# Optimization experiments

Measured on AMD Instinct MI355X. Metric: run time of the kernel, lower is better.

Reference implementation:

```python
import jax, jax.numpy as jnp
import numpy as np

SIZE = 1024
CODE_DIM = 256
B, H, W = 32, 32, 32


def setup_inputs() -> dict:
    key = jax.random.key(0)
    k1, k2 = jax.random.split(key)
    z = jax.random.normal(k1, (B, CODE_DIM, H, W), dtype=jnp.float32)
    embeddings = jax.random.normal(k2, (SIZE, CODE_DIM), dtype=jnp.float32)
    return {"z": z, "embeddings": embeddings}


def reference(z, embeddings):
    b, c, h, w = z.shape  # c == code_dim
    # (b, h, w, c) -> (N, c)
    flat = jnp.transpose(z, (0, 2, 3, 1)).reshape(-1, c)
    d = (
        jnp.sum(flat * flat, axis=-1, keepdims=True)
        - 2.0 * (flat @ embeddings.T)
        + jnp.sum(embeddings * embeddings, axis=-1)
    )
    idx = jnp.argmin(d, axis=-1)  # (N,)
    quantized = embeddings[idx].reshape(b, h, w, c)
    quantized = jnp.transpose(quantized, (0, 3, 1, 2))  # (b, c, h, w)
    straight_through = jax.lax.stop_gradient(quantized - z) + z
    return quantized, straight_through, idx.reshape(b, h, w)
```

## Files before the change

kernel.cpp:

```cpp
#include <hip/hip_runtime.h>

#define NPTS   32768
#define NCODES 1024
#define DIM    256
#define HWSZ   1024
#define CHW    (DIM*HWSZ)
#define QSZ    8388608

typedef __attribute__((ext_vector_type(8))) short short8;
typedef __attribute__((ext_vector_type(4))) float f32x4;

__device__ __forceinline__ void gload16(const void* g, void* l) {
    __builtin_amdgcn_global_load_lds((const __attribute__((address_space(1))) void*)g,
                                     (__attribute__((address_space(3))) void*)l,
                                     16, 0, 0);
}

__device__ __forceinline__ unsigned bf16_rne(float f) {
    unsigned u = __float_as_uint(f);
    return (u + 0x7fffu + ((u >> 16) & 1u)) >> 16;
}

__device__ __forceinline__ unsigned long long pack_di(float d, int code) {
    unsigned u = __float_as_uint(d);
    unsigned key = u ^ ((unsigned)((int)u >> 31) | 0x80000000u);
    return ((unsigned long long)key << 32) | (unsigned)code;
}

__global__ void k_prep(const float* __restrict__ z, const float* __restrict__ emb,
                       short* __restrict__ Xh, short* __restrict__ Xl,
                       short* __restrict__ Eh, short* __restrict__ El,
                       float* __restrict__ e2, unsigned long long* __restrict__ win) {
    int tid = threadIdx.x;
    if (blockIdx.x >= 2048) {
        int eb = blockIdx.x - 2048;
        int widx = eb * 256 + tid;
        if (widx < NPTS) win[widx] = ~0ull;
        int lane = tid & 63, w = tid >> 6;
        int k = eb * 4 + w;
        const float4 v = *reinterpret_cast<const float4*>(emb + k * DIM + lane * 4);
        float f[4] = {v.x, v.y, v.z, v.w};
        short h[4], l[4];
        double s = 0.0;
        #pragma unroll
        for (int i = 0; i < 4; ++i) {
            unsigned hb = bf16_rne(f[i]);
            float hf = __uint_as_float(hb << 16);
            h[i] = (short)hb;
            l[i] = (short)bf16_rne(f[i] - hf);
            s += (double)f[i] * f[i];
        }
        *reinterpret_cast<short4*>(Eh + k * DIM + lane * 4) = make_short4(h[0], h[1], h[2], h[3]);
        *reinterpret_cast<short4*>(El + k * DIM + lane * 4) = make_short4(l[0], l[1], l[2], l[3]);
        #pragma unroll
        for (int m = 32; m >= 1; m >>= 1) s += __shfl_xor(s, m);
        if (lane == 0) e2[k] = (float)s;
        return;
    }
    __shared__ float T[64][33];
    int blk = blockIdx.x;
    int b   = blk >> 6;
    int rem = blk & 63;
    int ht  = rem >> 1;
    int ch  = rem & 1;
    int hw0 = ht * 32;
    int n0  = b * HWSZ + hw0;
    int hq = tid & 7, cr = tid >> 3;
    int wp = tid >> 3, wc = tid & 7;
    const float* zp = z + b * CHW;
    #pragma unroll
    for (int cc2 = 0; cc2 < 2; ++cc2) {
        int c0 = (ch * 2 + cc2) * 64;
        if (cc2) __syncthreads();
        #pragma unroll
        for (int p = 0; p < 2; ++p) {
            int c = p * 32 + cr;
            float4 v = *reinterpret_cast<const float4*>(zp + (c0 + c) * HWSZ + hw0 + hq * 4);
            T[c][hq * 4 + 0] = v.x; T[c][hq * 4 + 1] = v.y;
            T[c][hq * 4 + 2] = v.z; T[c][hq * 4 + 3] = v.w;
        }
        __syncthreads();
        short8 hv, lv;
        #pragma unroll
        for (int k = 0; k < 8; ++k) {
            float f = T[wc * 8 + k][wp];
            unsigned hb = bf16_rne(f);
            float hf = __uint_as_float(hb << 16);
            hv[k] = (short)hb;
            lv[k] = (short)bf16_rne(f - hf);
        }
        *reinterpret_cast<short8*>(Xh + (n0 + wp) * DIM + c0 + wc * 8) = hv;
        *reinterpret_cast<short8*>(Xl + (n0 + wp) * DIM + c0 + wc * 8) = lv;
    }
}

__launch_bounds__(256, 4)
__global__ void k_dist(const short* __restrict__ Xh, const short* __restrict__ Xl,
                       const short* __restrict__ Eh, const short* __restrict__ El,
                       const float* __restrict__ e2, unsigned long long* __restrict__ win) {
    __shared__ __align__(16) short Ah[4096];
    __shared__ __align__(16) short Al[4096];
    __shared__ __align__(16) short Bh[4096];
    __shared__ __align__(16) short Bl[4096];
    __shared__ float sv[2][128];
    __shared__ int   si[2][128];

    const int tid = threadIdx.x;
    const int pt = blockIdx.x & 255;
    const int ct = blockIdx.x >> 8;
    const int n0 = pt * 128;
    const int c0 = ct * 128;

    const int w = tid >> 6, lane = tid & 63;
    const int wr = w >> 1, wc = w & 1;
    const int m16 = lane & 15, quad = lane >> 4;

    f32x4 acc[4][4];
    #pragma unroll
    for (int i = 0; i < 4; ++i)
        #pragma unroll
        for (int j = 0; j < 4; ++j) acc[i][j] = (f32x4){0.f, 0.f, 0.f, 0.f};

    const int r   = lane >> 2;
    const int swz = (((lane & 3) - ((lane >> 3) & 3)) & 3) * 8;
    const int ldsoff0 = (w * 16) * 64;
    const int ldsoff1 = (64 + w * 16) * 64;
    const int arow0 = (n0 + w * 16 + r) * DIM;
    const int arow1 = (n0 + 64 + w * 16 + r) * DIM;
    const int brow0 = (c0 + w * 16 + r) * DIM;
    const int brow1 = (c0 + 64 + w * 16 + r) * DIM;

    const int pq = ((quad + (m16 >> 1)) & 3) * 8;

    for (int t = 0; t < 8; ++t) {
        const int koff = t * 32 + swz;
        __syncthreads();
        gload16(Xh + arow0 + koff, (char*)Ah + ldsoff0);
        gload16(Xh + arow1 + koff, (char*)Ah + ldsoff1);
        gload16(Xl + arow0 + koff, (char*)Al + ldsoff0);
        gload16(Xl + arow1 + koff, (char*)Al + ldsoff1);
        gload16(Eh + brow0 + koff, (char*)Bh + ldsoff0);
        gload16(Eh + brow1 + koff, (char*)Bh + ldsoff1);
        gload16(El + brow0 + koff, (char*)Bl + ldsoff0);
        gload16(El + brow1 + koff, (char*)Bl + ldsoff1);
        __syncthreads();

        short8 ah[4], al[4], bh[4], bl[4];
        #pragma unroll
        for (int i = 0; i < 4; ++i) {
            int ar = (wr * 64 + i * 16 + m16) * 32 + pq;
            ah[i] = *(const short8*)&Ah[ar];
            al[i] = *(const short8*)&Al[ar];
        }
        #pragma unroll
        for (int j = 0; j < 4; ++j) {
            int br = (wc * 64 + j * 16 + m16) * 32 + pq;
            bh[j] = *(const short8*)&Bh[br];
            bl[j] = *(const short8*)&Bl[br];
        }
        #pragma unroll
        for (int i = 0; i < 4; ++i)
            #pragma unroll
            for (int j = 0; j < 4; ++j)
                acc[i][j] = __builtin_amdgcn_mfma_f32_16x16x32_bf16(ah[i], bh[j], acc[i][j], 0, 0, 0);
        #pragma unroll
        for (int i = 0; i < 4; ++i)
            #pragma unroll
            for (int j = 0; j < 4; ++j)
                acc[i][j] = __builtin_amdgcn_mfma_f32_16x16x32_bf16(al[i], bh[j], acc[i][j], 0, 0, 0);
        #pragma unroll
        for (int i = 0; i < 4; ++i)
            #pragma unroll
            for (int j = 0; j < 4; ++j)
                acc[i][j] = __builtin_amdgcn_mfma_f32_16x16x32_bf16(ah[i], bl[j], acc[i][j], 0, 0, 0);
    }

    float ecol[4];
    #pragma unroll
    for (int j = 0; j < 4; ++j) ecol[j] = e2[c0 + wc * 64 + j * 16 + m16];

    #pragma unroll
    for (int i = 0; i < 4; ++i) {
        #pragma unroll
        for (int rr = 0; rr < 4; ++rr) {
            float best = 3.4e38f; int bi = 0;
            #pragma unroll
            for (int j = 0; j < 4; ++j) {
                float d = fmaf(-2.f, acc[i][j][rr], ecol[j]);
                int code = c0 + wc * 64 + j * 16 + m16;
                if (d < best) { best = d; bi = code; }
            }
            #pragma unroll
            for (int m = 1; m < 16; m <<= 1) {
                float ov = __shfl_xor(best, m);
                int   oi = __shfl_xor(bi, m);
                if (ov < best || (ov == best && oi < bi)) { best = ov; bi = oi; }
            }
            if (m16 == 0) {
                int p = wr * 64 + i * 16 + quad * 4 + rr;
                sv[wc][p] = best; si[wc][p] = bi;
            }
        }
    }
    __syncthreads();
    if (tid < 128) {
        float v0 = sv[0][tid]; int i0 = si[0][tid];
        float v1 = sv[1][tid]; int i1 = si[1][tid];
        if (v1 < v0) { v0 = v1; i0 = i1; }
        atomicMin(win + n0 + tid, pack_di(v0, i0));
    }
}

__global__ void k_out(const float* __restrict__ z, const float* __restrict__ emb,
                      const unsigned long long* __restrict__ win,
                      float* __restrict__ out) {
    __shared__ float Q[32][129];
    __shared__ int sbi[32];
    int blk = blockIdx.x;
    int n0 = (blk >> 1) * 32;
    int ch = blk & 1;
    int tid = threadIdx.x;
    if (tid < 32) {
        int n = n0 + tid;
        int bi = (int)(unsigned)(win[n] & 0xFFFFFFFFull);
        sbi[tid] = bi;
        if (ch == 0) out[2 * QSZ + n] = (float)bi;
    }
    __syncthreads();
    {
        int pt = tid >> 3, co = tid & 7;
        const float* ep = emb + sbi[pt] * DIM + ch * 128;
        #pragma unroll
        for (int j = 0; j < 4; ++j) {
            int c = j * 32 + co * 4;
            float4 v = *reinterpret_cast<const float4*>(ep + c);
            Q[pt][c] = v.x; Q[pt][c + 1] = v.y; Q[pt][c + 2] = v.z; Q[pt][c + 3] = v.w;
        }
    }
    __syncthreads();
    int hq = tid & 7, cr = tid >> 3;
    int b = n0 >> 10, hw0 = (n0 & 1023) + hq * 4;
    #pragma unroll
    for (int it = 0; it < 4; ++it) {
        int cl = it * 32 + cr;
        int c  = ch * 128 + cl;
        int off = b * CHW + c * HWSZ + hw0;
        float4 zv = *reinterpret_cast<const float4*>(z + off);
        float4 q = make_float4(Q[hq * 4 + 0][cl], Q[hq * 4 + 1][cl],
                               Q[hq * 4 + 2][cl], Q[hq * 4 + 3][cl]);
        *reinterpret_cast<float4*>(out + off) = q;
        float4 st = make_float4((q.x - zv.x) + zv.x, (q.y - zv.y) + zv.y,
                                (q.z - zv.z) + zv.z, (q.w - zv.w) + zv.w);
        *reinterpret_cast<float4*>(out + QSZ + off) = st;
    }
}

extern "C" void kernel_launch(void* const* d_in, const int* in_sizes, int n_in,
                              void* d_out, int out_size, void* d_ws, size_t ws_size,
                              hipStream_t stream) {
    const float* z   = (const float*)d_in[0];
    const float* emb = (const float*)d_in[1];
    float* out = (float*)d_out;
    float* ws  = (float*)d_ws;

    short* Eh   = (short*)ws;
    short* El   = (short*)(ws + 131072);
    float* e2   = ws + 262144;
    unsigned long long* win = (unsigned long long*)(ws + 263168);

    short* Xh = (short*)out;
    short* Xl = (short*)(out + 4194304);

    hipLaunchKernelGGL(k_prep, dim3(2304), dim3(256), 0, stream, z, emb, Xh, Xl, Eh, El, e2, win);
    hipLaunchKernelGGL(k_dist, dim3(2048), dim3(256), 0, stream, Xh, Xl, Eh, El, e2, win);
    hipLaunchKernelGGL(k_out,  dim3(2048), dim3(256), 0, stream, z, emb, win, out);
}
```

Before: 164.9 us.

## Double-buffer A tile and prefetch next K-slice during distance GEMM

The point-embedding (A) LDS tiles are now double-buffered, so the next K-slice of A is prefetched while the current slice is consumed. Explicit vmcnt waits and raw barriers replace the two __syncthreads per iteration. The codebook (B) tile stays single-buffered and is still waited on every iteration, so only part of the load latency is hidden. The extra LDS cost lowers the launch-bounds occupancy target from 4 to 3 blocks per CU.

```diff
diff --git a/kernel.cpp b/kernel.cpp
--- a/kernel.cpp
+++ b/kernel.cpp
@@ -94,12 +94,12 @@
     }
 }
 
-__launch_bounds__(256, 4)
+__launch_bounds__(256, 3)
 __global__ void k_dist(const short* __restrict__ Xh, const short* __restrict__ Xl,
                        const short* __restrict__ Eh, const short* __restrict__ El,
                        const float* __restrict__ e2, unsigned long long* __restrict__ win) {
-    __shared__ __align__(16) short Ah[4096];
-    __shared__ __align__(16) short Al[4096];
+    __shared__ __align__(16) short Ah[2][4096];
+    __shared__ __align__(16) short Al[2][4096];
     __shared__ __align__(16) short Bh[4096];
     __shared__ __align__(16) short Bl[4096];
     __shared__ float sv[2][128];
@@ -132,25 +132,40 @@
 
     const int pq = ((quad + (m16 >> 1)) & 3) * 8;
 
+    #define STAGE_A(buf, t) do {                                      \
+        const int ka_ = (t) * 32 + swz;                               \
+        gload16(Xh + arow0 + ka_, (char*)Ah[buf] + ldsoff0);          \
+        gload16(Xh + arow1 + ka_, (char*)Ah[buf] + ldsoff1);          \
+        gload16(Xl + arow0 + ka_, (char*)Al[buf] + ldsoff0);          \
+        gload16(Xl + arow1 + ka_, (char*)Al[buf] + ldsoff1);          \
+    } while (0)
+    #define STAGE_B(t) do {                                           \
+        const int kb_ = (t) * 32 + swz;                               \
+        gload16(Eh + brow0 + kb_, (char*)Bh + ldsoff0);               \
+        gload16(Eh + brow1 + kb_, (char*)Bh + ldsoff1);               \
+        gload16(El + brow0 + kb_, (char*)Bl + ldsoff0);               \
+        gload16(El + brow1 + kb_, (char*)Bl + ldsoff1);               \
+    } while (0)
+
+    STAGE_A(0, 0);
+
     for (int t = 0; t < 8; ++t) {
-        const int koff = t * 32 + swz;
-        __syncthreads();
-        gload16(Xh + arow0 + koff, (char*)Ah + ldsoff0);
-        gload16(Xh + arow1 + koff, (char*)Ah + ldsoff1);
-        gload16(Xl + arow0 + koff, (char*)Al + ldsoff0);
-        gload16(Xl + arow1 + koff, (char*)Al + ldsoff1);
-        gload16(Eh + brow0 + koff, (char*)Bh + ldsoff0);
-        gload16(Eh + brow1 + koff, (char*)Bh + ldsoff1);
-        gload16(El + brow0 + koff, (char*)Bl + ldsoff0);
-        gload16(El + brow1 + koff, (char*)Bl + ldsoff1);
-        __syncthreads();
+        const int cur = t & 1;
+        __builtin_amdgcn_s_barrier();
+        STAGE_B(t);
+        if (t < 7) STAGE_A(cur ^ 1, t + 1);
+        if (t < 7) asm volatile("s_waitcnt vmcnt(4)" ::: "memory");
+        else       asm volatile("s_waitcnt vmcnt(0)" ::: "memory");
+        __builtin_amdgcn_s_barrier();
+        __builtin_amdgcn_sched_barrier(0);
 
         short8 ah[4], al[4], bh[4], bl[4];
+        const short* Ahc = Ah[cur]; const short* Alc = Al[cur];
         #pragma unroll
         for (int i = 0; i < 4; ++i) {
             int ar = (wr * 64 + i * 16 + m16) * 32 + pq;
-            ah[i] = *(const short8*)&Ah[ar];
-            al[i] = *(const short8*)&Al[ar];
+            ah[i] = *(const short8*)&Ahc[ar];
+            al[i] = *(const short8*)&Alc[ar];
         }
         #pragma unroll
         for (int j = 0; j < 4; ++j) {
@@ -174,6 +189,8 @@
             for (int j = 0; j < 4; ++j)
                 acc[i][j] = __builtin_amdgcn_mfma_f32_16x16x32_bf16(ah[i], bl[j], acc[i][j], 0, 0, 0);
     }
+    #undef STAGE_A
+    #undef STAGE_B
 
     float ecol[4];
     #pragma unroll
```

Result: slower. 169.1 us (+2.5%).

## Pre-swizzle operands into MFMA fragment layout and load directly from global

Applied to the files above, without the earlier changes.

The prep kernel now writes the bf16 hi/lo split of z and embeddings in a fragment-major layout, so each lane's short8 MFMA operand sits contiguously in memory. The distance kernel drops the LDS staging buffers and both per-iteration barriers, loading fragments straight from global memory into registers. MFMA sections are wrapped with s_setprio, and the occupancy hint drops from 4 to 3 waves per SIMD. The cost is that tiles shared by several waves are no longer reused through LDS, which means more global/L2 traffic and exposed load latency with no software prefetch.

```diff
diff --git a/kernel.cpp b/kernel.cpp
--- a/kernel.cpp
+++ b/kernel.cpp
@@ -10,12 +10,6 @@
 typedef __attribute__((ext_vector_type(8))) short short8;
 typedef __attribute__((ext_vector_type(4))) float f32x4;
 
-__device__ __forceinline__ void gload16(const void* g, void* l) {
-    __builtin_amdgcn_global_load_lds((const __attribute__((address_space(1))) void*)g,
-                                     (__attribute__((address_space(3))) void*)l,
-                                     16, 0, 0);
-}
-
 __device__ __forceinline__ unsigned bf16_rne(float f) {
     unsigned u = __float_as_uint(f);
     return (u + 0x7fffu + ((u >> 16) & 1u)) >> 16;
@@ -25,6 +19,11 @@
     unsigned u = __float_as_uint(d);
     unsigned key = u ^ ((unsigned)((int)u >> 31) | 0x80000000u);
     return ((unsigned long long)key << 32) | (unsigned)code;
+}
+
+__device__ __forceinline__ int fmoff(int n, int c) {
+    return ((((((n >> 7) * 2 + ((n >> 6) & 1)) * 8 + (c >> 5)) * 4 + ((n >> 4) & 3)) * 4
+             + ((c >> 3) & 3)) * 16 + (n & 15)) * 8 + (c & 7);
 }
 
 __global__ void k_prep(const float* __restrict__ z, const float* __restrict__ emb,
@@ -50,8 +49,9 @@
             l[i] = (short)bf16_rne(f[i] - hf);
             s += (double)f[i] * f[i];
         }
-        *reinterpret_cast<short4*>(Eh + k * DIM + lane * 4) = make_short4(h[0], h[1], h[2], h[3]);
-        *reinterpret_cast<short4*>(El + k * DIM + lane * 4) = make_short4(l[0], l[1], l[2], l[3]);
+        int eoff = fmoff(k, lane * 4);
+        *reinterpret_cast<short4*>(Eh + eoff) = make_short4(h[0], h[1], h[2], h[3]);
+        *reinterpret_cast<short4*>(El + eoff) = make_short4(l[0], l[1], l[2], l[3]);
         #pragma unroll
         for (int m = 32; m >= 1; m >>= 1) s += __shfl_xor(s, m);
         if (lane == 0) e2[k] = (float)s;
@@ -89,19 +89,16 @@
             hv[k] = (short)hb;
             lv[k] = (short)bf16_rne(f - hf);
         }
-        *reinterpret_cast<short8*>(Xh + (n0 + wp) * DIM + c0 + wc * 8) = hv;
-        *reinterpret_cast<short8*>(Xl + (n0 + wp) * DIM + c0 + wc * 8) = lv;
-    }
-}
-
-__launch_bounds__(256, 4)
+        int off = fmoff(n0 + wp, c0 + wc * 8);
+        *reinterpret_cast<short8*>(Xh + off) = hv;
+        *reinterpret_cast<short8*>(Xl + off) = lv;
+    }
+}
+
+__launch_bounds__(256, 3)
 __global__ void k_dist(const short* __restrict__ Xh, const short* __restrict__ Xl,
                        const short* __restrict__ Eh, const short* __restrict__ El,
                        const float* __restrict__ e2, unsigned long long* __restrict__ win) {
-    __shared__ __align__(16) short Ah[4096];
-    __shared__ __align__(16) short Al[4096];
-    __shared__ __align__(16) short Bh[4096];
-    __shared__ __align__(16) short Bl[4096];
     __shared__ float sv[2][128];
     __shared__ int   si[2][128];
 
@@ -121,43 +118,25 @@
         #pragma unroll
         for (int j = 0; j < 4; ++j) acc[i][j] = (f32x4){0.f, 0.f, 0.f, 0.f};
 
-    const int r   = lane >> 2;
-    const int swz = (((lane & 3) - ((lane >> 3) & 3)) & 3) * 8;
-    const int ldsoff0 = (w * 16) * 64;
-    const int ldsoff1 = (64 + w * 16) * 64;
-    const int arow0 = (n0 + w * 16 + r) * DIM;
-    const int arow1 = (n0 + 64 + w * 16 + r) * DIM;
-    const int brow0 = (c0 + w * 16 + r) * DIM;
-    const int brow1 = (c0 + 64 + w * 16 + r) * DIM;
-
-    const int pq = ((quad + (m16 >> 1)) & 3) * 8;
+    const short* Ahb = Xh + (pt * 2 + wr) * 16384 + lane * 8;
+    const short* Alb = Xl + (pt * 2 + wr) * 16384 + lane * 8;
+    const short* Bhb = Eh + (ct * 2 + wc) * 16384 + lane * 8;
+    const short* Blb = El + (ct * 2 + wc) * 16384 + lane * 8;
 
     for (int t = 0; t < 8; ++t) {
-        const int koff = t * 32 + swz;
-        __syncthreads();
-        gload16(Xh + arow0 + koff, (char*)Ah + ldsoff0);
-        gload16(Xh + arow1 + koff, (char*)Ah + ldsoff1);
-        gload16(Xl + arow0 + koff, (char*)Al + ldsoff0);
-        gload16(Xl + arow1 + koff, (char*)Al + ldsoff1);
-        gload16(Eh + brow0 + koff, (char*)Bh + ldsoff0);
-        gload16(Eh + brow1 + koff, (char*)Bh + ldsoff1);
-        gload16(El + brow0 + koff, (char*)Bl + ldsoff0);
-        gload16(El + brow1 + koff, (char*)Bl + ldsoff1);
-        __syncthreads();
-
+        const int to = t * 2048;
         short8 ah[4], al[4], bh[4], bl[4];
         #pragma unroll
         for (int i = 0; i < 4; ++i) {
-            int ar = (wr * 64 + i * 16 + m16) * 32 + pq;
-            ah[i] = *(const short8*)&Ah[ar];
-            al[i] = *(const short8*)&Al[ar];
+            ah[i] = *reinterpret_cast<const short8*>(Ahb + to + i * 512);
+            al[i] = *reinterpret_cast<const short8*>(Alb + to + i * 512);
         }
         #pragma unroll
         for (int j = 0; j < 4; ++j) {
-            int br = (wc * 64 + j * 16 + m16) * 32 + pq;
-            bh[j] = *(const short8*)&Bh[br];
-            bl[j] = *(const short8*)&Bl[br];
-        }
+            bh[j] = *reinterpret_cast<const short8*>(Bhb + to + j * 512);
+            bl[j] = *reinterpret_cast<const short8*>(Blb + to + j * 512);
+        }
+        __builtin_amdgcn_s_setprio(1);
         #pragma unroll
         for (int i = 0; i < 4; ++i)
             #pragma unroll
@@ -173,6 +152,7 @@
             #pragma unroll
             for (int j = 0; j < 4; ++j)
                 acc[i][j] = __builtin_amdgcn_mfma_f32_16x16x32_bf16(ah[i], bl[j], acc[i][j], 0, 0, 0);
+        __builtin_amdgcn_s_setprio(0);
     }
 
     float ecol[4];
```

Measured after the change: 163.3 us. Within noise of the previous version (-1.0%).
